# Performance work log

Hardware: AMD Instinct MI355X
Metric: run time of the kernel (lower is better)

The kernel has to match this reference:

```python
import jax, jax.numpy as jnp
import numpy as np

B, T, D = 4, 2048, 1024
H = 16
HD = D // H

def setup_inputs() -> dict:
    key = jax.random.key(0)
    ks = jax.random.split(key, 3)
    x = jax.random.normal(ks[0], (B, T, D), dtype=jnp.float32)
    w_qkv = jax.random.normal(ks[1], (D, 3 * D), dtype=jnp.float32) * (1.0 / np.sqrt(D))
    b_qkv = jnp.zeros((3 * D,), dtype=jnp.float32)
    w_proj = jax.random.normal(ks[2], (D, D), dtype=jnp.float32) * (1.0 / np.sqrt(D))
    b_proj = jnp.zeros((D,), dtype=jnp.float32)
    return {"x": x, "w_qkv": w_qkv, "b_qkv": b_qkv, "w_proj": w_proj, "b_proj": b_proj}

def reference(x, w_qkv, b_qkv, w_proj, b_proj):
    b, t, c = x.shape
    qkv = x @ w_qkv + b_qkv                      # [B,T,3D]
    qkv = qkv.reshape(b, t, 3, H, HD).transpose(2, 0, 3, 1, 4)  # [3,B,H,T,HD]
    q, k, v = qkv[0], qkv[1], qkv[2]
    scale = jnp.sqrt(jnp.asarray(HD, dtype=x.dtype))
    attn = jnp.einsum('bhqd,bhkd->bhqk', q, k) / scale  # [B,H,T,T]
    causal = jnp.tril(jnp.ones((t, t), dtype=bool))
    attn = jnp.where(causal[None, None], attn, -jnp.inf)
    attn = jax.nn.softmax(attn, axis=-1)
    out = jnp.einsum('bhqk,bhkd->bhqd', attn, v)        # [B,H,T,HD]
    out = out.transpose(0, 2, 1, 3).reshape(b, t, c)
    return out @ w_proj + b_proj
```

## Files before the change

kernel.cpp:

```cpp
#include <hip/hip_runtime.h>

typedef float f32x4 __attribute__((ext_vector_type(4)));
typedef __bf16 bf16x8 __attribute__((ext_vector_type(8)));

static __device__ __forceinline__ unsigned short f2bf(float f) {
    unsigned int u = __builtin_bit_cast(unsigned int, f);
    u += 0x7fffu + ((u >> 16) & 1u);
    return (unsigned short)(u >> 16);
}
static __device__ __forceinline__ unsigned short bfc(float f) {
    return __builtin_bit_cast(unsigned short, (__bf16)f);
}

#define QSC 0.18033688011112042f

typedef const __attribute__((address_space(1))) unsigned int gu32;
typedef __attribute__((address_space(3))) unsigned int lu32;
static __device__ __forceinline__ void gload_lds16(const unsigned short* g, unsigned short* l) {
    __builtin_amdgcn_global_load_lds((gu32*)g, (lu32*)l, 16, 0, 0);
}

__global__ __launch_bounds__(256)
void cvt_bf16(const float* __restrict__ in, unsigned short* __restrict__ out) {
    int i = blockIdx.x * 256 + threadIdx.x;
    const float4* p = (const float4*)in + (size_t)i * 2;
    float4 a = p[0], b = p[1];
    union { unsigned short s[8]; uint4 v; } u;
    u.s[0] = f2bf(a.x); u.s[1] = f2bf(a.y); u.s[2] = f2bf(a.z); u.s[3] = f2bf(a.w);
    u.s[4] = f2bf(b.x); u.s[5] = f2bf(b.y); u.s[6] = f2bf(b.z); u.s[7] = f2bf(b.w);
    ((uint4*)out)[i] = u.v;
}

__global__ __launch_bounds__(256)
void transpose_w(const float* __restrict__ w, unsigned short* __restrict__ wT,
                 int K, int N) {
    __shared__ unsigned short Lt[64][65];
    const int k0 = blockIdx.x * 64, n0 = blockIdx.y * 64;
    const int t = threadIdx.x;
    const int r = t >> 4, c4 = (t & 15) * 4;
    #pragma unroll
    for (int i = 0; i < 4; i++) {
        int rr = r + i * 16;
        float4 v = *(const float4*)(w + (k0 + rr) * N + n0 + c4);
        Lt[rr][c4 + 0] = f2bf(v.x); Lt[rr][c4 + 1] = f2bf(v.y);
        Lt[rr][c4 + 2] = f2bf(v.z); Lt[rr][c4 + 3] = f2bf(v.w);
    }
    __syncthreads();
    const int rn = t >> 3, ks = (t & 7) * 8;
    #pragma unroll
    for (int i = 0; i < 2; i++) {
        int rr = rn + i * 32;
        unsigned short tmp[8];
        #pragma unroll
        for (int j = 0; j < 8; j++) tmp[j] = Lt[ks + j][rr];
        *(uint4*)(wT + (n0 + rr) * K + k0 + ks) = *(const uint4*)tmp;
    }
}

__global__ __launch_bounds__(256)
void qkv_gemm2(const unsigned short* __restrict__ A,
               const unsigned short* __restrict__ Bt,
               const float* __restrict__ bias,
               unsigned short* __restrict__ q_ws,
               unsigned short* __restrict__ k_ws,
               unsigned short* __restrict__ vT_ws)
{
    const int K = 1024;
    __shared__ unsigned short Al[2][128 * 32];
    __shared__ unsigned short Bl[2][128 * 32];
    const int tid = threadIdx.x;
    const int lane = tid & 63, w = tid >> 6;
    const int l15 = lane & 15, lhi = lane >> 4;
    const int m0 = blockIdx.x * 128, n0 = blockIdx.y * 128;
    const int wm = (w >> 1) * 64, wn = (w & 1) * 64;

    const int srow = w * 32 + (lane >> 2);
    const int sg = ((lane & 3) ^ ((lane >> 3) & 3)) * 8;
    const unsigned short* ga = A + (size_t)(m0 + srow) * K + sg;
    const unsigned short* gb = Bt + (size_t)(n0 + srow) * K + sg;
    const int lofs = w * 32 * 32;

    const int rc = (lhi ^ ((l15 >> 1) & 3)) * 8;

    f32x4 acc[4][4] = {};

    gload_lds16(ga, &Al[0][lofs]);
    gload_lds16(ga + 16 * K, &Al[0][lofs + 512]);
    gload_lds16(gb, &Bl[0][lofs]);
    gload_lds16(gb + 16 * K, &Bl[0][lofs + 512]);
    __syncthreads();

    int cur = 0;
    for (int k0 = 0; k0 < K; k0 += 32) {
        const int nxt = cur ^ 1;
        if (k0 + 32 < K) {
            gload_lds16(ga + k0 + 32,          &Al[nxt][lofs]);
            gload_lds16(ga + k0 + 32 + 16 * K, &Al[nxt][lofs + 512]);
            gload_lds16(gb + k0 + 32,          &Bl[nxt][lofs]);
            gload_lds16(gb + k0 + 32 + 16 * K, &Bl[nxt][lofs + 512]);
        }
        bf16x8 af[4], bfr[4];
        #pragma unroll
        for (int m = 0; m < 4; m++)
            af[m] = *(const bf16x8*)(&Al[cur][(wm + m * 16 + l15) * 32 + rc]);
        #pragma unroll
        for (int n = 0; n < 4; n++)
            bfr[n] = *(const bf16x8*)(&Bl[cur][(wn + n * 16 + l15) * 32 + rc]);
        __builtin_amdgcn_s_setprio(1);
        #pragma unroll
        for (int m = 0; m < 4; m++)
            #pragma unroll
            for (int n = 0; n < 4; n++)
                acc[m][n] = __builtin_amdgcn_mfma_f32_16x16x32_bf16(af[m], bfr[n], acc[m][n], 0, 0, 0);
        __builtin_amdgcn_s_setprio(0);
        __syncthreads();
        cur = nxt;
    }

    #pragma unroll
    for (int n = 0; n < 4; n++) {
        int col = n0 + wn + n * 16 + l15;
        float bv = bias[col];
        int which = col >> 10;
        int d = col & 1023;
        int h = d >> 6, hd = d & 63;
        if (which == 2) {
            #pragma unroll
            for (int m = 0; m < 4; m++) {
                int row0 = m0 + wm + m * 16 + lhi * 4;
                int b = row0 >> 11, t0 = row0 & 2047;
                ushort4 pk;
                pk.x = f2bf(acc[m][n][0] + bv);
                pk.y = f2bf(acc[m][n][1] + bv);
                pk.z = f2bf(acc[m][n][2] + bv);
                pk.w = f2bf(acc[m][n][3] + bv);
                *(ushort4*)(&vT_ws[((size_t)(b * 16 + h) * 64 + hd) * 2048 + t0]) = pk;
            }
        } else {
            #pragma unroll
            for (int m = 0; m < 4; m++) {
                #pragma unroll
                for (int j = 0; j < 4; j++) {
                    int row = m0 + wm + m * 16 + lhi * 4 + j;
                    int b = row >> 11, t = row & 2047;
                    float val = acc[m][n][j] + bv;
                    int bh = b * 16 + h;
                    if (which == 0) q_ws[(bh * 2048 + t) * 64 + hd] = f2bf(val * QSC);
                    else            k_ws[(bh * 2048 + t) * 64 + hd] = f2bf(val);
                }
            }
        }
    }
}

#define LKK 72

__global__ __launch_bounds__(512, 4)
void attn_fwd(const unsigned short* __restrict__ q_ws,
              const unsigned short* __restrict__ k_ws,
              const unsigned short* __restrict__ vT_ws,
              unsigned short* __restrict__ attn_ws)
{
    __shared__ unsigned short Kb[2][64 * LKK];
    __shared__ unsigned short Vb[2][64 * LKK];
    __shared__ unsigned short Pl[8][16 * 64];

    const int bh = blockIdx.x;
    const int p  = blockIdx.y;
    const int b = bh >> 4, h = bh & 15;
    const int tid = threadIdx.x;
    const int lane = tid & 63, wid = tid >> 6;
    const int l15 = lane & 15, lhi = lane >> 4;
    const int tbase = bh * 2048;
    const float NINF = -__builtin_inff();

    const int r0 = tid >> 3;
    const int c0 = (tid & 7) * 8;
    const unsigned short* kg = k_ws + (size_t)(tbase + r0) * 64 + c0;
    const unsigned short* vg = vT_ws + ((size_t)bh * 64 + r0) * 2048 + c0;

    unsigned short* Pw = &Pl[wid][0];
    const int xr = l15 & 7;

    bf16x8 ones;
    #pragma unroll
    for (int z = 0; z < 8; z++) ones[z] = (__bf16)1.0f;

    #pragma unroll 1
    for (int seg = 0; seg < 2; ++seg) {
        const int qb = seg ? p : 15 - p;
        const int q0 = qb * 128;
        const int qrow = q0 + wid * 16;
        const int nkv = 2 * (qb + 1);

        bf16x8 qf[2];
        #pragma unroll
        for (int ks = 0; ks < 2; ks++)
            qf[ks] = *(const bf16x8*)(q_ws + (size_t)(tbase + qrow + l15) * 64 + ks * 32 + lhi * 8);

        f32x4 o[4] = {};
        f32x4 osum = {0.f, 0.f, 0.f, 0.f};

        {
            uint4 ka = *(const uint4*)(kg);
            uint4 va = *(const uint4*)(vg);
            *(uint4*)(&Kb[0][r0 * LKK + c0]) = ka;
            *(uint4*)(&Vb[0][r0 * LKK + c0]) = va;
        }
        __syncthreads();

        int cur = 0;
        for (int kb = 0; kb < nkv; ++kb) {
            const int k0 = kb * 64;
            const int knx = (kb + 1 < nkv ? kb + 1 : kb) * 64;
            uint4 ka = *(const uint4*)(kg + (size_t)knx * 64);
            uint4 va = *(const uint4*)(vg + knx);

            if (k0 <= qrow + 15) {
                f32x4 s[4] = {};
                __builtin_amdgcn_s_setprio(1);
                #pragma unroll
                for (int ks = 0; ks < 2; ks++) {
                    bf16x8 kf[4];
                    #pragma unroll
                    for (int n = 0; n < 4; n++)
                        kf[n] = *(const bf16x8*)(&Kb[cur][(n * 16 + l15) * LKK + ks * 32 + lhi * 8]);
                    #pragma unroll
                    for (int n = 0; n < 4; n++)
                        s[n] = __builtin_amdgcn_mfma_f32_16x16x32_bf16(kf[n], qf[ks], s[n], 0, 0, 0);
                }
                __builtin_amdgcn_s_setprio(0);
                if (k0 + 63 > qrow) {
                    int qg = qrow + l15;
                    #pragma unroll
                    for (int n = 0; n < 4; n++) {
                        int kgl = k0 + n * 16 + lhi * 4;
                        #pragma unroll
                        for (int j = 0; j < 4; j++)
                            s[n][j] = (kgl + j <= qg) ? s[n][j] : NINF;
                    }
                }
                #pragma unroll
                for (int n = 0; n < 4; n++)
                    #pragma unroll
                    for (int j = 0; j < 4; j++)
                        s[n][j] = exp2f(s[n][j]);
                #pragma unroll
                for (int n = 0; n < 4; n++) {
                    ushort4 pk;
                    pk.x = bfc(s[n][0]); pk.y = bfc(s[n][1]);
                    pk.z = bfc(s[n][2]); pk.w = bfc(s[n][3]);
                    int chunk = (2 * n + (lhi >> 1)) ^ xr;
                    *(ushort4*)(&Pw[l15 * 64 + chunk * 8 + (lhi & 1) * 4]) = pk;
                }
                __builtin_amdgcn_s_setprio(1);
                #pragma unroll
                for (int ks = 0; ks < 2; ks++) {
                    int chunk = (4 * ks + lhi) ^ xr;
                    bf16x8 pf = *(const bf16x8*)(&Pw[l15 * 64 + chunk * 8]);
                    bf16x8 vf[4];
                    #pragma unroll
                    for (int nd = 0; nd < 4; nd++)
                        vf[nd] = *(const bf16x8*)(&Vb[cur][(nd * 16 + l15) * LKK + ks * 32 + lhi * 8]);
                    #pragma unroll
                    for (int nd = 0; nd < 4; nd++)
                        o[nd] = __builtin_amdgcn_mfma_f32_16x16x32_bf16(pf, vf[nd], o[nd], 0, 0, 0);
                    osum = __builtin_amdgcn_mfma_f32_16x16x32_bf16(pf, ones, osum, 0, 0, 0);
                }
                __builtin_amdgcn_s_setprio(0);
            }
            *(uint4*)(&Kb[cur ^ 1][r0 * LKK + c0]) = ka;
            *(uint4*)(&Vb[cur ^ 1][r0 * LKK + c0]) = va;
            __syncthreads();
            cur ^= 1;
        }
        #pragma unroll
        for (int j = 0; j < 4; j++) {
            float inv = 1.0f / osum[j];
            int t = qrow + lhi * 4 + j;
            #pragma unroll
            for (int nd = 0; nd < 4; nd++) {
                int d = nd * 16 + l15;
                attn_ws[((size_t)(b * 2048 + t) * 16 + h) * 64 + d] = f2bf(o[nd][j] * inv);
            }
        }
    }
}

__global__ __launch_bounds__(256)
void proj_gemm2(const unsigned short* __restrict__ A,
                const unsigned short* __restrict__ Bt,
                const float* __restrict__ bias, float* __restrict__ out)
{
    const int K = 1024, N = 1024;
    __shared__ unsigned short Al[2][128 * 32];
    __shared__ unsigned short Bl[2][128 * 32];
    const int tid = threadIdx.x;
    const int lane = tid & 63, w = tid >> 6;
    const int l15 = lane & 15, lhi = lane >> 4;
    const int m0 = blockIdx.x * 128, n0 = blockIdx.y * 128;
    const int wm = (w >> 1) * 64, wn = (w & 1) * 64;

    const int srow = w * 32 + (lane >> 2);
    const int sg = ((lane & 3) ^ ((lane >> 3) & 3)) * 8;
    const unsigned short* ga = A + (size_t)(m0 + srow) * K + sg;
    const unsigned short* gb = Bt + (size_t)(n0 + srow) * K + sg;
    const int lofs = w * 32 * 32;

    const int rc = (lhi ^ ((l15 >> 1) & 3)) * 8;

    f32x4 acc[4][4] = {};

    gload_lds16(ga, &Al[0][lofs]);
    gload_lds16(ga + 16 * K, &Al[0][lofs + 512]);
    gload_lds16(gb, &Bl[0][lofs]);
    gload_lds16(gb + 16 * K, &Bl[0][lofs + 512]);
    __syncthreads();

    int cur = 0;
    for (int k0 = 0; k0 < K; k0 += 32) {
        const int nxt = cur ^ 1;
        if (k0 + 32 < K) {
            gload_lds16(ga + k0 + 32,          &Al[nxt][lofs]);
            gload_lds16(ga + k0 + 32 + 16 * K, &Al[nxt][lofs + 512]);
            gload_lds16(gb + k0 + 32,          &Bl[nxt][lofs]);
            gload_lds16(gb + k0 + 32 + 16 * K, &Bl[nxt][lofs + 512]);
        }
        bf16x8 af[4], bfr[4];
        #pragma unroll
        for (int m = 0; m < 4; m++)
            af[m] = *(const bf16x8*)(&Al[cur][(wm + m * 16 + l15) * 32 + rc]);
        #pragma unroll
        for (int n = 0; n < 4; n++)
            bfr[n] = *(const bf16x8*)(&Bl[cur][(wn + n * 16 + l15) * 32 + rc]);
        __builtin_amdgcn_s_setprio(1);
        #pragma unroll
        for (int m = 0; m < 4; m++)
            #pragma unroll
            for (int n = 0; n < 4; n++)
                acc[m][n] = __builtin_amdgcn_mfma_f32_16x16x32_bf16(af[m], bfr[n], acc[m][n], 0, 0, 0);
        __builtin_amdgcn_s_setprio(0);
        __syncthreads();
        cur = nxt;
    }

    #pragma unroll
    for (int n = 0; n < 4; n++) {
        int col = n0 + wn + n * 16 + l15;
        float bv = bias[col];
        #pragma unroll
        for (int m = 0; m < 4; m++)
            #pragma unroll
            for (int j = 0; j < 4; j++) {
                int row = m0 + wm + m * 16 + lhi * 4 + j;
                out[row * N + col] = acc[m][n][j] + bv;
            }
    }
}

extern "C" void kernel_launch(void* const* d_in, const int* in_sizes, int n_in,
                              void* d_out, int out_size, void* d_ws, size_t ws_size,
                              hipStream_t stream)
{
    const float* x      = (const float*)d_in[0];
    const float* w_qkv  = (const float*)d_in[1];
    const float* b_qkv  = (const float*)d_in[2];
    const float* w_proj = (const float*)d_in[3];
    const float* b_proj = (const float*)d_in[4];
    float* out = (float*)d_out;

    const size_t SEG = (size_t)8 * 1024 * 1024;
    unsigned short* q_ws    = (unsigned short*)d_ws;
    unsigned short* k_ws    = q_ws + SEG;
    unsigned short* vT_ws   = k_ws + SEG;
    unsigned short* attn_ws = vT_ws + SEG;

    unsigned short* x_bf   = (unsigned short*)d_out;
    unsigned short* wqkvT  = x_bf + SEG;
    unsigned short* wprojT = q_ws;

    cvt_bf16<<<4096, 256, 0, stream>>>(x, x_bf);
    transpose_w<<<dim3(16, 48), 256, 0, stream>>>(w_qkv, wqkvT, 1024, 3072);
    qkv_gemm2<<<dim3(64, 24), 256, 0, stream>>>(x_bf, wqkvT, b_qkv, q_ws, k_ws, vT_ws);
    attn_fwd<<<dim3(64, 8), 512, 0, stream>>>(q_ws, k_ws, vT_ws, attn_ws);
    transpose_w<<<dim3(16, 16), 256, 0, stream>>>(w_proj, wprojT, 1024, 1024);
    proj_gemm2<<<dim3(64, 8), 256, 0, stream>>>(attn_ws, wprojT, b_proj, out);
}
```

Baseline: 175.9 us.

## Give each attention wave 32 query rows and drop the two-segment pairing

```diff
diff --git a/kernel.cpp b/kernel.cpp
--- a/kernel.cpp
+++ b/kernel.cpp
@@ -163,10 +163,11 @@
 {
     __shared__ unsigned short Kb[2][64 * LKK];
     __shared__ unsigned short Vb[2][64 * LKK];
-    __shared__ unsigned short Pl[8][16 * 64];
+    __shared__ unsigned short Pl[8][2][16 * 64];
 
     const int bh = blockIdx.x;
-    const int p  = blockIdx.y;
+    const int slot = blockIdx.y;
+    const int qb = (slot < 4) ? slot : (11 - slot);
     const int b = bh >> 4, h = bh & 15;
     const int tid = threadIdx.x;
     const int lane = tid & 63, wid = tid >> 6;
@@ -179,109 +180,120 @@
     const unsigned short* kg = k_ws + (size_t)(tbase + r0) * 64 + c0;
     const unsigned short* vg = vT_ws + ((size_t)bh * 64 + r0) * 2048 + c0;
 
-    unsigned short* Pw = &Pl[wid][0];
     const int xr = l15 & 7;
 
     bf16x8 ones;
     #pragma unroll
     for (int z = 0; z < 8; z++) ones[z] = (__bf16)1.0f;
 
-    #pragma unroll 1
-    for (int seg = 0; seg < 2; ++seg) {
-        const int qb = seg ? p : 15 - p;
-        const int q0 = qb * 128;
-        const int qrow = q0 + wid * 16;
-        const int nkv = 2 * (qb + 1);
-
-        bf16x8 qf[2];
+    const int qrow = qb * 256 + wid * 32;
+    const int nkv = 4 * (qb + 1);
+
+    bf16x8 qf[2][2];
+    #pragma unroll
+    for (int m = 0; m < 2; m++)
         #pragma unroll
         for (int ks = 0; ks < 2; ks++)
-            qf[ks] = *(const bf16x8*)(q_ws + (size_t)(tbase + qrow + l15) * 64 + ks * 32 + lhi * 8);
-
-        f32x4 o[4] = {};
-        f32x4 osum = {0.f, 0.f, 0.f, 0.f};
-
-        {
-            uint4 ka = *(const uint4*)(kg);
-            uint4 va = *(const uint4*)(vg);
-            *(uint4*)(&Kb[0][r0 * LKK + c0]) = ka;
-            *(uint4*)(&Vb[0][r0 * LKK + c0]) = va;
-        }
-        __syncthreads();
-
-        int cur = 0;
-        for (int kb = 0; kb < nkv; ++kb) {
-            const int k0 = kb * 64;
-            const int knx = (kb + 1 < nkv ? kb + 1 : kb) * 64;
-            uint4 ka = *(const uint4*)(kg + (size_t)knx * 64);
-            uint4 va = *(const uint4*)(vg + knx);
-
-            if (k0 <= qrow + 15) {
-                f32x4 s[4] = {};
-                __builtin_amdgcn_s_setprio(1);
-                #pragma unroll
-                for (int ks = 0; ks < 2; ks++) {
-                    bf16x8 kf[4];
+            qf[m][ks] = *(const bf16x8*)(q_ws + (size_t)(tbase + qrow + m * 16 + l15) * 64 + ks * 32 + lhi * 8);
+
+    f32x4 o[2][4] = {};
+    f32x4 osum[2] = {};
+
+    {
+        uint4 ka = *(const uint4*)(kg);
+        uint4 va = *(const uint4*)(vg);
+        *(uint4*)(&Kb[0][r0 * LKK + c0]) = ka;
+        *(uint4*)(&Vb[0][r0 * LKK + c0]) = va;
+    }
+    __syncthreads();
+
+    int cur = 0;
+    for (int kb = 0; kb < nkv; ++kb) {
+        const int k0 = kb * 64;
+        const int knx = (kb + 1 < nkv ? kb + 1 : kb) * 64;
+        uint4 ka = *(const uint4*)(kg + (size_t)knx * 64);
+        uint4 va = *(const uint4*)(vg + knx);
+
+        if (k0 <= qrow + 31) {
+            f32x4 s[2][4] = {};
+            __builtin_amdgcn_s_setprio(1);
+            #pragma unroll
+            for (int ks = 0; ks < 2; ks++) {
+                bf16x8 kf[4];
+                #pragma unroll
+                for (int n = 0; n < 4; n++)
+                    kf[n] = *(const bf16x8*)(&Kb[cur][(n * 16 + l15) * LKK + ks * 32 + lhi * 8]);
+                #pragma unroll
+                for (int m = 0; m < 2; m++)
                     #pragma unroll
                     for (int n = 0; n < 4; n++)
-                        kf[n] = *(const bf16x8*)(&Kb[cur][(n * 16 + l15) * LKK + ks * 32 + lhi * 8]);
-                    #pragma unroll
-                    for (int n = 0; n < 4; n++)
-                        s[n] = __builtin_amdgcn_mfma_f32_16x16x32_bf16(kf[n], qf[ks], s[n], 0, 0, 0);
-                }
-                __builtin_amdgcn_s_setprio(0);
-                if (k0 + 63 > qrow) {
-                    int qg = qrow + l15;
+                        s[m][n] = __builtin_amdgcn_mfma_f32_16x16x32_bf16(kf[n], qf[m][ks], s[m][n], 0, 0, 0);
+            }
+            __builtin_amdgcn_s_setprio(0);
+            if (k0 + 63 > qrow) {
+                #pragma unroll
+                for (int m = 0; m < 2; m++) {
+                    int qg = qrow + m * 16 + l15;
                     #pragma unroll
                     for (int n = 0; n < 4; n++) {
                         int kgl = k0 + n * 16 + lhi * 4;
                         #pragma unroll
                         for (int j = 0; j < 4; j++)
-                            s[n][j] = (kgl + j <= qg) ? s[n][j] : NINF;
+                            s[m][n][j] = (kgl + j <= qg) ? s[m][n][j] : NINF;
                     }
                 }
+            }
+            #pragma unroll
+            for (int m = 0; m < 2; m++)
                 #pragma unroll
                 for (int n = 0; n < 4; n++)
                     #pragma unroll
                     for (int j = 0; j < 4; j++)
-                        s[n][j] = exp2f(s[n][j]);
+                        s[m][n][j] = exp2f(s[m][n][j]);
+            #pragma unroll
+            for (int m = 0; m < 2; m++)
                 #pragma unroll
                 for (int n = 0; n < 4; n++) {
                     ushort4 pk;
-                    pk.x = bfc(s[n][0]); pk.y = bfc(s[n][1]);
-                    pk.z = bfc(s[n][2]); pk.w = bfc(s[n][3]);
+                    pk.x = bfc(s[m][n][0]); pk.y = bfc(s[m][n][1]);
+                    pk.z = bfc(s[m][n][2]); pk.w = bfc(s[m][n][3]);
                     int chunk = (2 * n + (lhi >> 1)) ^ xr;
-                    *(ushort4*)(&Pw[l15 * 64 + chunk * 8 + (lhi & 1) * 4]) = pk;
+                    *(ushort4*)(&Pl[wid][m][l15 * 64 + chunk * 8 + (lhi & 1) * 4]) = pk;
                 }
-                __builtin_amdgcn_s_setprio(1);
-                #pragma unroll
-                for (int ks = 0; ks < 2; ks++) {
-                    int chunk = (4 * ks + lhi) ^ xr;
-                    bf16x8 pf = *(const bf16x8*)(&Pw[l15 * 64 + chunk * 8]);
-                    bf16x8 vf[4];
+            __builtin_amdgcn_s_setprio(1);
+            #pragma unroll
+            for (int ks = 0; ks < 2; ks++) {
+                int chunk = (4 * ks + lhi) ^ xr;
+                bf16x8 vf[4];
+                #pragma unroll
+                for (int nd = 0; nd < 4; nd++)
+                    vf[nd] = *(const bf16x8*)(&Vb[cur][(nd * 16 + l15) * LKK + ks * 32 + lhi * 8]);
+                #pragma unroll
+                for (int m = 0; m < 2; m++) {
+                    bf16x8 pf = *(const bf16x8*)(&Pl[wid][m][l15 * 64 + chunk * 8]);
                     #pragma unroll
                     for (int nd = 0; nd < 4; nd++)
-                        vf[nd] = *(const bf16x8*)(&Vb[cur][(nd * 16 + l15) * LKK + ks * 32 + lhi * 8]);
-                    #pragma unroll
-                    for (int nd = 0; nd < 4; nd++)
-                        o[nd] = __builtin_amdgcn_mfma_f32_16x16x32_bf16(pf, vf[nd], o[nd], 0, 0, 0);
-                    osum = __builtin_amdgcn_mfma_f32_16x16x32_bf16(pf, ones, osum, 0, 0, 0);
+                        o[m][nd] = __builtin_amdgcn_mfma_f32_16x16x32_bf16(pf, vf[nd], o[m][nd], 0, 0, 0);
+                    osum[m] = __builtin_amdgcn_mfma_f32_16x16x32_bf16(pf, ones, osum[m], 0, 0, 0);
                 }
-                __builtin_amdgcn_s_setprio(0);
-            }
-            *(uint4*)(&Kb[cur ^ 1][r0 * LKK + c0]) = ka;
-            *(uint4*)(&Vb[cur ^ 1][r0 * LKK + c0]) = va;
-            __syncthreads();
-            cur ^= 1;
+            }
+            __builtin_amdgcn_s_setprio(0);
         }
+        *(uint4*)(&Kb[cur ^ 1][r0 * LKK + c0]) = ka;
+        *(uint4*)(&Vb[cur ^ 1][r0 * LKK + c0]) = va;
+        __syncthreads();
+        cur ^= 1;
+    }
+    #pragma unroll
+    for (int m = 0; m < 2; m++) {
         #pragma unroll
         for (int j = 0; j < 4; j++) {
-            float inv = 1.0f / osum[j];
-            int t = qrow + lhi * 4 + j;
+            float inv = 1.0f / osum[m][j];
+            int t = qrow + m * 16 + lhi * 4 + j;
             #pragma unroll
             for (int nd = 0; nd < 4; nd++) {
                 int d = nd * 16 + l15;
-                attn_ws[((size_t)(b * 2048 + t) * 16 + h) * 64 + d] = f2bf(o[nd][j] * inv);
+                attn_ws[((size_t)(b * 2048 + t) * 16 + h) * 64 + d] = f2bf(o[m][nd][j] * inv);
             }
         }
     }
```

Result: slower. 213.4 us (+21.4%).
